# Kernel tuning notes

Measured on AMD Instinct MI355X. Metric: run time of the kernel, lower is better.

Reference implementation:

```python
import jax, jax.numpy as jnp
import numpy as np

TEMP = 0.07
MOMENTUM = 0.2
K = 8192          # number of sampled negatives per row
NUM_CLASSES = 1000
B, N, D = 256, 32768, 2048
NEG_INF = -1e30


def _gumbel(key, shape):
    u = jax.random.uniform(key, shape, minval=1e-6, maxval=1.0)
    return -jnp.log(-jnp.log(u))


def setup_inputs() -> dict:
    key = jax.random.key(0)
    k1, k2, k3, k4, k5 = jax.random.split(key, 5)
    f = jax.random.normal(k1, (B, D), dtype=jnp.float32)
    f_nv = jax.random.normal(k2, (B, D), dtype=jnp.float32)
    # warmed-up memory bank (the real module L2-normalizes rows on update)
    features = jax.random.normal(k3, (N, D), dtype=jnp.float32)
    features = features / jnp.linalg.norm(features, axis=1, keepdims=True)
    labels = jax.random.randint(k4, (N,), 0, NUM_CLASSES)
    indexes = jax.random.randint(k5, (B,), 0, N)
    return {"f": f, "f_nv": f_nv, "features": features,
            "labels": labels, "indexes": indexes}


def reference(f, f_nv, features, labels, indexes):
    rkey = jax.random.key(42)
    kg1, kg2, kg3 = jax.random.split(rkey, 3)
    k = features                                   # [N, D] memory bank snapshot
    bsz = f.shape[0]

    # l_pos = <f_nv_i, k[indexes_i]>
    l_pos = jnp.sum(f_nv * k[indexes], axis=1, keepdims=True)   # [B, 1]

    mat = jnp.matmul(f, k.T)                       # [B, N]
    mat_sim = jnp.matmul(f_nv, k.T)                # [B, N]

    batch_labels = labels[indexes]                 # [B]
    pos_mask = labels[None, :] == batch_labels[:, None]         # [B, N]

    # torch.randperm-based sampling -> vectorized masked Gumbel sampling.
    # argmax of gumbel restricted to mask = uniform draw from masked set;
    # top-K of gumbel restricted to complement = K draws w/o replacement.
    g1 = _gumbel(kg1, (bsz, k.shape[0]))
    g2 = _gumbel(kg2, (bsz, k.shape[0]))
    g3 = _gumbel(kg3, (bsz, k.shape[0]))

    pos_idx_wogan = jnp.argmax(jnp.where(pos_mask, g1, NEG_INF), axis=1)
    positives_wogan = jnp.take_along_axis(mat, pos_idx_wogan[:, None], axis=1)  # [B,1]

    pos_idx = jnp.argmax(jnp.where(pos_mask, g2, NEG_INF), axis=1)
    positives = jnp.take_along_axis(mat_sim, pos_idx[:, None], axis=1)          # [B,1]

    _, neg_idx = jax.lax.top_k(jnp.where(pos_mask, NEG_INF, g3), K)             # [B,K]
    negatives = jnp.take_along_axis(mat_sim, neg_idx, axis=1)                   # [B,K]

    def ce_target0(logits):
        # CrossEntropyLoss with all targets == 0
        return -jax.nn.log_softmax(logits, axis=1)[:, 0].mean()

    self_out = jnp.concatenate([l_pos, negatives], axis=1) / TEMP
    inter_out = jnp.concatenate([positives, negatives], axis=1) / TEMP
    inter_out_wogan = jnp.concatenate([positives_wogan, negatives], axis=1) / TEMP

    memory_loss = ce_target0(self_out) + ce_target0(inter_out) + ce_target0(inter_out_wogan)

    # no-grad momentum update of the bank (F.normalize uses eps=1e-12)
    upd = MOMENTUM * k[indexes] + (1.0 - MOMENTUM) * f
    upd = upd / jnp.maximum(jnp.linalg.norm(upd, axis=1, keepdims=True), 1e-12)
    new_features = jax.lax.stop_gradient(features.at[indexes].set(upd))

    return memory_loss, new_features
```

## Files before the change

kernel.cpp:

```cpp
#include <hip/hip_runtime.h>
#include <stdint.h>

#define TEMP      0.07f
#define BATCH     256
#define NROWS     32768
#define DIM       2048
#define KNEG      8192

typedef __attribute__((ext_vector_type(8))) short bf16x8;
typedef __attribute__((ext_vector_type(4))) float f32x4;

__host__ __device__ inline void tf2x32(uint32_t ka, uint32_t kb,
                                       uint32_t x0, uint32_t x1,
                                       uint32_t& o0, uint32_t& o1) {
  uint32_t ks2 = ka ^ kb ^ 0x1BD11BDAu;
#define TFR(r) { x0 += x1; x1 = (x1 << r) | (x1 >> (32 - r)); x1 ^= x0; }
  x0 += ka; x1 += kb;
  TFR(13) TFR(15) TFR(26) TFR(6)
  x0 += kb;  x1 += ks2 + 1u;
  TFR(17) TFR(29) TFR(16) TFR(24)
  x0 += ks2; x1 += ka + 2u;
  TFR(13) TFR(15) TFR(26) TFR(6)
  x0 += ka;  x1 += kb + 3u;
  TFR(17) TFR(29) TFR(16) TFR(24)
  x0 += kb;  x1 += ks2 + 4u;
  TFR(13) TFR(15) TFR(26) TFR(6)
  x0 += ks2; x1 += ka + 5u;
#undef TFR
  o0 = x0; o1 = x1;
}

__device__ inline uint32_t ubits_at(uint32_t ka, uint32_t kb, uint32_t q) {
  uint32_t a, b; tf2x32(ka, kb, 0u, q, a, b);
  return (a ^ b) >> 9;
}

__device__ inline float block_sum(float v, float* sm) {
  __syncthreads();
  const int lane = threadIdx.x & 63;
  const int w = threadIdx.x >> 6;
  const int nw = blockDim.x >> 6;
  for (int o = 32; o; o >>= 1) v += __shfl_down(v, o, 64);
  if (lane == 0) sm[w] = v;
  __syncthreads();
  if (w == 0) {
    float x = (lane < nw) ? sm[lane] : 0.f;
    for (int o = 8; o; o >>= 1) x += __shfl_down(x, o, 64);
    if (lane == 0) sm[0] = x;
  }
  __syncthreads();
  return sm[0];
}

__device__ inline uint32_t pk2(float a, float b) {
  uint32_t ua = __float_as_uint(a), ub = __float_as_uint(b);
  ua = (ua + 0x7FFFu + ((ua >> 16) & 1u)) >> 16;
  ub = (ub + 0x7FFFu + ((ub >> 16) & 1u)) >> 16;
  return ua | (ub << 16);
}

__global__ __launch_bounds__(256) void cvtA(const float* __restrict__ A,
                                            uint32_t* __restrict__ Abf) {
  const int t = threadIdx.x;
  const int w = blockIdx.x * 4 + (t >> 6);
  const int l = t & 63;
  const int mt = w >> 6, kt = w & 63;
  const float* src = &A[(size_t)(mt * 16 + (l & 15)) * DIM + kt * 32 + (l >> 4) * 8];
  float4 f0 = *(const float4*)src;
  float4 f1 = *(const float4*)(src + 4);
  *(uint4*)(Abf + (size_t)w * 256 + l * 4) =
      make_uint4(pk2(f0.x, f0.y), pk2(f0.z, f0.w), pk2(f1.x, f1.y), pk2(f1.z, f1.w));
}

__device__ inline void gll16(const float* g, float* l) {
  __builtin_amdgcn_global_load_lds(
      (const __attribute__((address_space(1))) uint32_t*)g,
      (__attribute__((address_space(3))) uint32_t*)l, 16, 0, 0);
}

__global__ __launch_bounds__(256, 4) void mega(
    const uint32_t* __restrict__ Abf,
    const float* __restrict__ Bfeat,
    float* __restrict__ C,
    float* __restrict__ outF,
    int skip) {
  __shared__ float Bs[64 * 64];
  const int role = blockIdx.x % 3;
  const int g = blockIdx.x / 3;
  const int t = threadIdx.x;

  if (role < 2) {
    const int r0 = g * 64 + role * 32;
    const float* src = Bfeat + (size_t)r0 * DIM;
    float* dst = outF + (size_t)r0 * DIM;
    const int total4 = 32 * DIM / 4;
#pragma unroll 4
    for (int i = t; i < total4; i += 256) {
      const int gr = r0 + (i >> 9);
      f32x4 v = *(const f32x4*)(src + (size_t)i * 4);
      if (gr >= skip)
        __builtin_nontemporal_store(v, (f32x4*)(dst + (size_t)i * 4));
    }
    return;
  }

  const int l = t & 63, w = t >> 6;
  f32x4 acc[4][4] = {};

  for (int t0 = 0; t0 < DIM / 64; ++t0) {
    __syncthreads();
#pragma unroll
    for (int i = 0; i < 4; ++i) {
      const int ii = w * 4 + i;
      const int r = 4 * ii + (l >> 4);
      const int gs = (l & 15) ^ (r & 7);
      gll16(&Bfeat[(size_t)(g * 64 + r) * DIM + t0 * 64 + gs * 4],
            &Bs[ii * 256]);
    }
    __syncthreads();
#pragma unroll
    for (int kk = 0; kk < 2; ++kk) {
      bf16x8 af[4];
#pragma unroll
      for (int m = 0; m < 4; ++m)
        af[m] = *(const bf16x8*)(Abf +
            ((size_t)((w * 4 + m) * 64 + t0 * 2 + kk) * 64 + l) * 4);
      bf16x8 bfr[4];
#pragma unroll
      for (int n = 0; n < 4; ++n) {
        const int row = n * 16 + (l & 15);
        const int b2 = 2 * (kk * 4 + (l >> 4));
        const int s = row & 7;
        f32x4 lo = *(const f32x4*)&Bs[row * 64 + (b2 ^ s) * 4];
        f32x4 hi = *(const f32x4*)&Bs[row * 64 + ((b2 + 1) ^ s) * 4];
        uint32_t c0, c1, c2, c3;
        asm("v_cvt_pk_bf16_f32 %0, %1, %2" : "=v"(c0) : "v"(lo[0]), "v"(lo[1]));
        asm("v_cvt_pk_bf16_f32 %0, %1, %2" : "=v"(c1) : "v"(lo[2]), "v"(lo[3]));
        asm("v_cvt_pk_bf16_f32 %0, %1, %2" : "=v"(c2) : "v"(hi[0]), "v"(hi[1]));
        asm("v_cvt_pk_bf16_f32 %0, %1, %2" : "=v"(c3) : "v"(hi[2]), "v"(hi[3]));
        union { uint32_t u[4]; bf16x8 b; } cv;
        cv.u[0] = c0; cv.u[1] = c1; cv.u[2] = c2; cv.u[3] = c3;
        bfr[n] = cv.b;
      }
#pragma unroll
      for (int m = 0; m < 4; ++m)
#pragma unroll
        for (int n = 0; n < 4; ++n)
          acc[m][n] = __builtin_amdgcn_mfma_f32_16x16x32_bf16(
              af[m], bfr[n], acc[m][n], 0, 0, 0);
    }
  }

#pragma unroll
  for (int m = 0; m < 4; ++m)
#pragma unroll
    for (int n = 0; n < 4; ++n) {
      const int row0 = w * 64 + m * 16 + (l >> 4) * 4;
      const int col = g * 64 + n * 16 + (l & 15);
#pragma unroll
      for (int r = 0; r < 4; ++r)
        C[(size_t)(row0 + r) * NROWS + col] = acc[m][n][r];
    }
}

__global__ __launch_bounds__(1024) void sample_loss(
    const float* __restrict__ f, const float* __restrict__ f_nv,
    const float* __restrict__ features, const int* __restrict__ labels,
    const int* __restrict__ indexes, const float* __restrict__ mat_sim,
    float* __restrict__ row_loss,
    uint32_t k1a, uint32_t k1b, uint32_t k2a, uint32_t k2b,
    uint32_t k3a, uint32_t k3b) {
  __shared__ uint32_t keys[NROWS];
  __shared__ uint32_t hist4[4][256];
  __shared__ uint32_t hist[256];
  __shared__ unsigned long long am1, am2;
  __shared__ int tie_j[128];
  __shared__ int tie_cnt;
  __shared__ float sred[16];
  __shared__ float swm[16], sws[16];
  __shared__ uint32_t bc_prefix, bc_rem;
  __shared__ int blab_s;

  const int t = threadIdx.x;
  const int i = blockIdx.x;
  const size_t mbase = (size_t)i * NROWS;

  if (t == 0) {
    blab_s = labels[indexes[i]];
    am1 = 0ull; am2 = 0ull; tie_cnt = 0;
  }
  ((uint32_t*)hist4)[t] = 0u;
  __syncthreads();
  const int blab = blab_s;
  const int hsel = t >> 8;

#pragma unroll 2
  for (int s = 0; s < NROWS / 1024; ++s) {
    int j = t + 1024 * s;
    uint32_t q = (uint32_t)i * NROWS + (uint32_t)j;
    int lab = labels[j];
    uint32_t key;
    if (lab == blab) {
      key = 0u;
      unsigned long long lo = (unsigned long long)(uint32_t)(NROWS - 1 - j);
      uint32_t u1 = ubits_at(k1a, k1b, q);
      uint32_t u2 = ubits_at(k2a, k2b, q);
      atomicMax(&am1, ((unsigned long long)u1 << 32) | lo);
      atomicMax(&am2, ((unsigned long long)u2 << 32) | lo);
    } else {
      key = ubits_at(k3a, k3b, q);
    }
    keys[j] = key;
    atomicAdd(&hist4[hsel][key >> 15], 1u);
  }
  __syncthreads();

  const int jw = NROWS - 1 - (int)(unsigned)(am1 & 0xFFFFFFFFull);
  const int jp = NROWS - 1 - (int)(unsigned)(am2 & 0xFFFFFFFFull);

  const int bank = indexes[i];
  float d1 = 0.f, d2 = 0.f, d3 = 0.f;
  for (int d = t; d < DIM; d += 1024) {
    float fnv = f_nv[(size_t)i * DIM + d];
    d1 += fnv * features[(size_t)bank * DIM + d];
    d2 += f[(size_t)i * DIM + d] * features[(size_t)jw * DIM + d];
    d3 += fnv * features[(size_t)jp * DIM + d];
  }
  const float l_pos = block_sum(d1, sred);
  const float posw  = block_sum(d2, sred);
  const float posv  = block_sum(d3, sred);

  uint32_t prefix = 0, remaining = KNEG;
  const int shifts[3] = {15, 7, 0};
  const int nbits[3]  = {8, 8, 7};
  for (int p = 0; p < 3; ++p) {
    const int sh = shifts[p];
    const int nb = 1 << nbits[p];
    if (p) {
      ((uint32_t*)hist4)[t] = 0u;
      __syncthreads();
      for (int s = 0; s < NROWS / 1024; ++s) {
        int j = t + 1024 * s;
        uint32_t k = keys[j];
        if ((k >> (sh + nbits[p])) == prefix)
          atomicAdd(&hist4[hsel][(k >> sh) & (uint32_t)(nb - 1)], 1u);
      }
    }
    __syncthreads();
    if (t < nb) hist[t] = hist4[0][t] + hist4[1][t] + hist4[2][t] + hist4[3][t];
    __syncthreads();
    if (t == 0) {
      uint32_t c = 0; int b = nb - 1;
      for (;; --b) {
        c += hist[b];
        if (c >= remaining || b == 0) break;
      }
      bc_prefix = (prefix << nbits[p]) | (uint32_t)b;
      bc_rem = remaining - (c - hist[b]);
    }
    __syncthreads();
    prefix = bc_prefix; remaining = bc_rem;
  }
  const uint32_t T = prefix;
  const uint32_t need = remaining;

  float m = -INFINITY, ssum = 0.f;
  for (int s = 0; s < NROWS / 1024; ++s) {
    int j = t + 1024 * s;
    uint32_t k = keys[j];
    if (k > T) {
      float v = mat_sim[mbase + j] / TEMP;
      if (v <= m) ssum += expf(v - m);
      else { ssum = ssum * expf(m - v) + 1.0f; m = v; }
    } else if (k == T) {
      int p = atomicAdd(&tie_cnt, 1);
      if (p < 128) tie_j[p] = j;
    }
  }
  for (int o = 32; o; o >>= 1) {
    float m2 = __shfl_down(m, o, 64);
    float s2 = __shfl_down(ssum, o, 64);
    if (m2 > m) { ssum = ssum * expf(m - m2) + s2; m = m2; }
    else if (m2 != -INFINITY) ssum += s2 * expf(m2 - m);
  }
  if ((t & 63) == 0) { swm[t >> 6] = m; sws[t >> 6] = ssum; }
  __syncthreads();
  if (t < 64) {
    float mm = (t < 16) ? swm[t] : -INFINITY;
    float ss = (t < 16) ? sws[t] : 0.f;
    for (int o = 8; o; o >>= 1) {
      float m2 = __shfl_down(mm, o, 64);
      float s2 = __shfl_down(ss, o, 64);
      if (m2 > mm) { ss = ss * expf(mm - m2) + s2; mm = m2; }
      else if (m2 != -INFINITY) ss += s2 * expf(m2 - mm);
    }
    if (t == 0) { swm[0] = mm; sws[0] = ss; }
  }
  __syncthreads();

  if (t == 0) {
    float M = swm[0], S = sws[0];
    int tc = tie_cnt;
    if (tc <= 128) {
      for (int a2 = 1; a2 < tc; ++a2) {
        int v = tie_j[a2]; int b2 = a2 - 1;
        while (b2 >= 0 && tie_j[b2] > v) { tie_j[b2 + 1] = tie_j[b2]; --b2; }
        tie_j[b2 + 1] = v;
      }
      for (uint32_t r = 0; r < need; ++r) {
        float v = mat_sim[mbase + tie_j[r]] / TEMP;
        if (v <= M) S += expf(v - M);
        else { S = S * expf(M - v) + 1.0f; M = v; }
      }
    } else {
      uint32_t taken = 0;
      for (int j = 0; j < NROWS && taken < need; ++j) {
        if (keys[j] == T) {
          float v = mat_sim[mbase + j] / TEMP;
          if (v <= M) S += expf(v - M);
          else { S = S * expf(M - v) + 1.0f; M = v; }
          ++taken;
        }
      }
    }
    float lp = l_pos / TEMP, pv = posv / TEMP, pw = posw / TEMP;
    float L = 0.f;
    { float X = fmaxf(M, lp); L += X + logf(expf(lp - X) + S * expf(M - X)) - lp; }
    { float X = fmaxf(M, pv); L += X + logf(expf(pv - X) + S * expf(M - X)) - pv; }
    { float X = fmaxf(M, pw); L += X + logf(expf(pw - X) + S * expf(M - X)) - pw; }
    row_loss[i] = L;
  }
}

__global__ void finalize_loss(const float* __restrict__ row_loss,
                              float* __restrict__ out) {
  __shared__ float sm[4];
  int t = threadIdx.x;
  float v = row_loss[t];
  for (int o = 32; o; o >>= 1) v += __shfl_down(v, o, 64);
  if ((t & 63) == 0) sm[t >> 6] = v;
  __syncthreads();
  if (t == 0) out[0] = (sm[0] + sm[1] + sm[2] + sm[3]) * (1.0f / BATCH);
}

__global__ void copy_front(const float* __restrict__ src,
                           float* __restrict__ dst, int n4) {
  int idx = blockIdx.x * blockDim.x + threadIdx.x;
  int stride = gridDim.x * blockDim.x;
  for (int i = idx; i < n4; i += stride) {
    f32x4 v = *(const f32x4*)&src[(size_t)i * 4];
    float* d = &dst[(size_t)i * 4];
    d[0] = v[0]; d[1] = v[1]; d[2] = v[2]; d[3] = v[3];
  }
}

__global__ __launch_bounds__(256) void update_rows(
    const float* __restrict__ f, const float* __restrict__ features,
    const int* __restrict__ indexes, float* __restrict__ outF) {
  __shared__ float sred[16];
  const int i = blockIdx.x;
  const int row = indexes[i];
  for (int i2 = i + 1; i2 < BATCH; ++i2)
    if (indexes[i2] == row) return;
  const int t = threadIdx.x;
  float ss = 0.f;
  for (int d = t; d < DIM; d += 256) {
    float u = 0.2f * features[(size_t)row * DIM + d] + 0.8f * f[(size_t)i * DIM + d];
    ss += u * u;
  }
  ss = block_sum(ss, sred);
  float nrm = fmaxf(sqrtf(ss), 1e-12f);
  for (int d = t; d < DIM; d += 256) {
    float u = 0.2f * features[(size_t)row * DIM + d] + 0.8f * f[(size_t)i * DIM + d];
    outF[(size_t)row * DIM + d] = u / nrm;
  }
}

extern "C" void kernel_launch(void* const* d_in, const int* in_sizes, int n_in,
                              void* d_out, int out_size, void* d_ws, size_t ws_size,
                              hipStream_t stream) {
  (void)in_sizes; (void)n_in; (void)out_size;
  const float* f        = (const float*)d_in[0];
  const float* f_nv     = (const float*)d_in[1];
  const float* features = (const float*)d_in[2];
  const int*   labels   = (const int*)d_in[3];
  const int*   indexes  = (const int*)d_in[4];
  float* out = (float*)d_out;

  const size_t need = ((size_t)BATCH * NROWS + 256 + 262144) * sizeof(float);
  float* mat_sim;
  float* row_loss;
  uint32_t* Abf;
  int skip_rows;
  bool use_ws = (d_ws != nullptr) && (ws_size >= need);
  if (use_ws) {
    mat_sim = (float*)d_ws;
    row_loss = mat_sim + (size_t)BATCH * NROWS;
    Abf = (uint32_t*)(row_loss + 256);
    skip_rows = 0;
  } else {
    mat_sim = out + 4;
    row_loss = mat_sim + (size_t)BATCH * NROWS;
    Abf = (uint32_t*)(row_loss + 256);
    skip_rows = 4352;
  }

  uint32_t c[6];
  { uint32_t a, b;
    tf2x32(0u, 42u, 0u, 0u, a, b); c[0] = a; c[1] = b;
    tf2x32(0u, 42u, 0u, 1u, a, b); c[2] = a; c[3] = b;
    tf2x32(0u, 42u, 0u, 2u, a, b); c[4] = a; c[5] = b; }

  cvtA<<<dim3(256), dim3(256), 0, stream>>>(f_nv, Abf);
  mega<<<dim3(3 * NROWS / 64), dim3(256), 0, stream>>>(
      Abf, features, mat_sim, out + 1, skip_rows);
  sample_loss<<<dim3(BATCH), dim3(1024), 0, stream>>>(
      f, f_nv, features, labels, indexes, mat_sim, row_loss,
      c[0], c[1], c[2], c[3], c[4], c[5]);
  finalize_loss<<<dim3(1), dim3(256), 0, stream>>>(row_loss, out);
  if (!use_ws) {
    copy_front<<<dim3(2048), dim3(256), 0, stream>>>(
        features, out + 1, 4352 * DIM / 4);
  }
  update_rows<<<dim3(BATCH), dim3(256), 0, stream>>>(f, features, indexes, out + 1);
}
```

Measured before the change: 284.5 us.

## Split GEMM K dimension in two with partial outputs summed in sampler

```diff
diff --git a/kernel.cpp b/kernel.cpp
--- a/kernel.cpp
+++ b/kernel.cpp
@@ -81,12 +81,12 @@
 __global__ __launch_bounds__(256, 4) void mega(
     const uint32_t* __restrict__ Abf,
     const float* __restrict__ Bfeat,
-    float* __restrict__ C,
+    float* __restrict__ matp,
     float* __restrict__ outF,
     int skip) {
   __shared__ float Bs[64 * 64];
-  const int role = blockIdx.x % 3;
-  const int g = blockIdx.x / 3;
+  const int role = blockIdx.x & 3;
+  const int g = blockIdx.x >> 2;
   const int t = threadIdx.x;
 
   if (role < 2) {
@@ -99,22 +99,24 @@
       const int gr = r0 + (i >> 9);
       f32x4 v = *(const f32x4*)(src + (size_t)i * 4);
       if (gr >= skip)
-        __builtin_nontemporal_store(v, (f32x4*)(dst + (size_t)i * 4));
+        *(f32x4*)(dst + (size_t)i * 4) = v;
     }
     return;
   }
 
+  const int kh = role - 2;
   const int l = t & 63, w = t >> 6;
   f32x4 acc[4][4] = {};
 
-  for (int t0 = 0; t0 < DIM / 64; ++t0) {
+  for (int t0 = 0; t0 < 16; ++t0) {
+    const int k0 = kh * 1024 + t0 * 64;
     __syncthreads();
 #pragma unroll
     for (int i = 0; i < 4; ++i) {
       const int ii = w * 4 + i;
       const int r = 4 * ii + (l >> 4);
       const int gs = (l & 15) ^ (r & 7);
-      gll16(&Bfeat[(size_t)(g * 64 + r) * DIM + t0 * 64 + gs * 4],
+      gll16(&Bfeat[(size_t)(g * 64 + r) * DIM + k0 + gs * 4],
             &Bs[ii * 256]);
     }
     __syncthreads();
@@ -124,7 +126,7 @@
 #pragma unroll
       for (int m = 0; m < 4; ++m)
         af[m] = *(const bf16x8*)(Abf +
-            ((size_t)((w * 4 + m) * 64 + t0 * 2 + kk) * 64 + l) * 4);
+            ((size_t)((w * 4 + m) * 64 + kh * 32 + t0 * 2 + kk) * 64 + l) * 4);
       bf16x8 bfr[4];
 #pragma unroll
       for (int n = 0; n < 4; ++n) {
@@ -151,6 +153,7 @@
     }
   }
 
+  float* Cp = matp + (size_t)kh * BATCH * NROWS;
 #pragma unroll
   for (int m = 0; m < 4; ++m)
 #pragma unroll
@@ -159,14 +162,15 @@
       const int col = g * 64 + n * 16 + (l & 15);
 #pragma unroll
       for (int r = 0; r < 4; ++r)
-        C[(size_t)(row0 + r) * NROWS + col] = acc[m][n][r];
+        Cp[(size_t)(row0 + r) * NROWS + col] = acc[m][n][r];
     }
 }
 
 __global__ __launch_bounds__(1024) void sample_loss(
     const float* __restrict__ f, const float* __restrict__ f_nv,
     const float* __restrict__ features, const int* __restrict__ labels,
-    const int* __restrict__ indexes, const float* __restrict__ mat_sim,
+    const int* __restrict__ indexes,
+    const float* __restrict__ p0, const float* __restrict__ p1,
     float* __restrict__ row_loss,
     uint32_t k1a, uint32_t k1b, uint32_t k2a, uint32_t k2b,
     uint32_t k3a, uint32_t k3b) {
@@ -269,7 +273,7 @@
     int j = t + 1024 * s;
     uint32_t k = keys[j];
     if (k > T) {
-      float v = mat_sim[mbase + j] / TEMP;
+      float v = (p0[mbase + j] + p1[mbase + j]) / TEMP;
       if (v <= m) ssum += expf(v - m);
       else { ssum = ssum * expf(m - v) + 1.0f; m = v; }
     } else if (k == T) {
@@ -308,7 +312,7 @@
         tie_j[b2 + 1] = v;
       }
       for (uint32_t r = 0; r < need; ++r) {
-        float v = mat_sim[mbase + tie_j[r]] / TEMP;
+        float v = (p0[mbase + tie_j[r]] + p1[mbase + tie_j[r]]) / TEMP;
         if (v <= M) S += expf(v - M);
         else { S = S * expf(M - v) + 1.0f; M = v; }
       }
@@ -316,7 +320,7 @@
       uint32_t taken = 0;
       for (int j = 0; j < NROWS && taken < need; ++j) {
         if (keys[j] == T) {
-          float v = mat_sim[mbase + j] / TEMP;
+          float v = (p0[mbase + j] + p1[mbase + j]) / TEMP;
           if (v <= M) S += expf(v - M);
           else { S = S * expf(M - v) + 1.0f; M = v; }
           ++taken;
@@ -387,23 +391,22 @@
   const int*   indexes  = (const int*)d_in[4];
   float* out = (float*)d_out;
 
-  const size_t need = ((size_t)BATCH * NROWS + 256 + 262144) * sizeof(float);
-  float* mat_sim;
+  const size_t n_mat = (size_t)BATCH * NROWS;
+  const size_t n_scratch = 2 * n_mat + 256 + 262144;
+  float* matp;
   float* row_loss;
   uint32_t* Abf;
   int skip_rows;
-  bool use_ws = (d_ws != nullptr) && (ws_size >= need);
+  bool use_ws = (d_ws != nullptr) && (ws_size >= n_scratch * sizeof(float));
   if (use_ws) {
-    mat_sim = (float*)d_ws;
-    row_loss = mat_sim + (size_t)BATCH * NROWS;
-    Abf = (uint32_t*)(row_loss + 256);
+    matp = (float*)d_ws;
     skip_rows = 0;
   } else {
-    mat_sim = out + 4;
-    row_loss = mat_sim + (size_t)BATCH * NROWS;
-    Abf = (uint32_t*)(row_loss + 256);
-    skip_rows = 4352;
-  }
+    matp = out + 4;
+    skip_rows = 8321;
+  }
+  row_loss = matp + 2 * n_mat;
+  Abf = (uint32_t*)(row_loss + 256);
 
   uint32_t c[6];
   { uint32_t a, b;
@@ -412,15 +415,15 @@
     tf2x32(0u, 42u, 0u, 2u, a, b); c[4] = a; c[5] = b; }
 
   cvtA<<<dim3(256), dim3(256), 0, stream>>>(f_nv, Abf);
-  mega<<<dim3(3 * NROWS / 64), dim3(256), 0, stream>>>(
-      Abf, features, mat_sim, out + 1, skip_rows);
+  mega<<<dim3(4 * NROWS / 64), dim3(256), 0, stream>>>(
+      Abf, features, matp, out + 1, skip_rows);
   sample_loss<<<dim3(BATCH), dim3(1024), 0, stream>>>(
-      f, f_nv, features, labels, indexes, mat_sim, row_loss,
+      f, f_nv, features, labels, indexes, matp, matp + n_mat, row_loss,
       c[0], c[1], c[2], c[3], c[4], c[5]);
   finalize_loss<<<dim3(1), dim3(256), 0, stream>>>(row_loss, out);
   if (!use_ws) {
     copy_front<<<dim3(2048), dim3(256), 0, stream>>>(
-        features, out + 1, 4352 * DIM / 4);
+        features, out + 1, 8321 * DIM / 4);
   }
   update_rows<<<dim3(BATCH), dim3(256), 0, stream>>>(f, features, indexes, out + 1);
 }
```

After: 301.4 us. 1.06x slower.
